# Kernel tuning notes

Hardware: AMD Instinct MI355X
Metric: run time of the kernel (lower is better)

Reference implementation:

```python
import jax, jax.numpy as jnp
import numpy as np
import math

H = 2048        # hidden_size
I = 8192        # intermediate_size
NH = 16         # num_heads
NKV = 4         # num_kv_heads
HD = 128        # head_dim
RD = 128        # rope_dim
THETA = 1000000.0
C = 8192        # context_length
EPS = 1e-6


def setup_inputs() -> dict:
    key = jax.random.key(0)
    ks = jax.random.split(key, 12)
    s = 0.02
    w = lambda k, shape: jax.random.normal(k, shape, jnp.float32) * s
    inp = {
        "hidden_states": jax.random.normal(ks[0], (1, 1, H), jnp.float32),
        "current_pos": jnp.array([4000], dtype=jnp.int32),
        "causal_mask": jnp.zeros((1, 1, 1, C), jnp.float32),
        "Wq": w(ks[1], (NH * HD * 2, H)),
        "Wk": w(ks[2], (NKV * HD, H)),
        "Wv": w(ks[3], (NKV * HD, H)),
        "Wo": w(ks[4], (H, NH * HD)),
        "q_norm": jnp.ones((HD,), jnp.float32),
        "k_norm": jnp.ones((HD,), jnp.float32),
        "ln1_w": jnp.ones((H,), jnp.float32),
        "ln2_w": jnp.ones((H,), jnp.float32),
        "W_gate": w(ks[5], (I, H)),
        "W_up": w(ks[6], (I, H)),
        "W_down": w(ks[7], (H, I)),
        "kv_cache": jax.random.normal(ks[8], (2, NKV, C, HD), jnp.float32) * 0.5,
    }
    inv_freq = 1.0 / (THETA ** (jnp.arange(0, RD, 2, dtype=jnp.float32) / RD))
    freqs = jnp.arange(C, dtype=jnp.float32)[:, None] * inv_freq[None, :]  # [C, RD/2]
    inp["rope_cos"] = jnp.cos(freqs)
    inp["rope_sin"] = jnp.sin(freqs)
    return inp


def _rms(x, w):
    return x * jax.lax.rsqrt(jnp.mean(x * x, axis=-1, keepdims=True) + EPS) * w


def _rope(x, cos, sin):
    # x: [heads, head_dim]; cos/sin: [RD/2]
    half = RD // 2
    x1, x2, xp = x[:, :half], x[:, half:RD], x[:, RD:]
    return jnp.concatenate([x1 * cos - x2 * sin, x2 * cos + x1 * sin, xp], axis=-1)


def reference(hidden_states, current_pos, causal_mask, Wq, Wk, Wv, Wo,
              q_norm, k_norm, ln1_w, ln2_w, W_gate, W_up, W_down,
              kv_cache, rope_cos, rope_sin):
    residual = hidden_states
    h = _rms(hidden_states, ln1_w)[0, 0]                  # [H]
    qg = (Wq @ h).reshape(NH, 2 * HD)
    q, gate = qg[:, :HD], qg[:, HD:]
    k = (Wk @ h).reshape(NKV, HD)
    v = (Wv @ h).reshape(NKV, HD)
    q = _rms(q, q_norm)
    k = _rms(k, k_norm)
    p = current_pos[0]
    cos, sin = rope_cos[p], rope_sin[p]
    q = _rope(q, cos, sin)
    k = _rope(k, cos, sin)
    z = jnp.int32(0)
    kc = jax.lax.dynamic_update_slice(kv_cache[0], k[:, None, :], (z, p, z))  # [NKV, C, HD]
    vc = jax.lax.dynamic_update_slice(kv_cache[1], v[:, None, :], (z, p, z))
    groups = NH // NKV
    k_exp = jnp.repeat(kc, groups, axis=0)                # [NH, C, HD]
    v_exp = jnp.repeat(vc, groups, axis=0)
    scale = 1.0 / math.sqrt(HD)
    scores = jnp.einsum('hd,hcd->hc', q, k_exp) * scale + causal_mask.reshape(1, C)
    attn = jax.nn.softmax(scores, axis=-1)
    attn_out = jnp.einsum('hc,hcd->hd', attn, v_exp) * jax.nn.sigmoid(gate)
    out = (Wo @ attn_out.reshape(NH * HD)).reshape(1, 1, H)
    x = residual + out
    h2 = _rms(x, ln2_w)
    ffn = (jax.nn.silu(h2 @ W_gate.T) * (h2 @ W_up.T)) @ W_down.T
    return x + ffn
```

## Files before the change

### kernel.cpp

```cpp
#include <hip/hip_runtime.h>

#define H 2048
#define NH 16
#define NKV 4
#define HD 128
#define CTX 8192
#define IDIM 8192
#define EPS 1e-6f
#define SCALE 0.08838834764831845f

__device__ __forceinline__ float wave_sum(float x){
#pragma unroll
    for(int o=32;o>0;o>>=1) x += __shfl_xor(x,o,64);
    return x;
}
__device__ __forceinline__ float wave_max(float x){
#pragma unroll
    for(int o=32;o>0;o>>=1) x = fmaxf(x,__shfl_xor(x,o,64));
    return x;
}
__device__ __forceinline__ void keep4(const float4& v){
    asm volatile("" :: "v"(v.x), "v"(v.y), "v"(v.z), "v"(v.w));
}
__device__ __forceinline__ void stage16(const float* g, float* l){
    __builtin_amdgcn_global_load_lds(
        (const __attribute__((address_space(1))) void*)g,
        (__attribute__((address_space(3))) void*)l, 16, 0, 0);
}

__global__ __launch_bounds__(512) void k_qkv(const float* __restrict__ Wq,
                                             const float* __restrict__ Wk,
                                             const float* __restrict__ Wv,
                                             const float* __restrict__ hs,
                                             const float* __restrict__ ln1,
                                             float* __restrict__ qg,
                                             float* __restrict__ kvec,
                                             float* __restrict__ vvec){
    __shared__ __align__(16) float hw[H];
    __shared__ __align__(16) float wlds[8*2048];
    __shared__ float red[8];
    int tid = threadIdx.x, wid = tid>>6, lane = tid&63;
    int row = blockIdx.x*8 + wid;
    const float* wr; float* op;
    if(row < 4096)      { wr = Wq + (size_t)row*H;        op = qg   + row; }
    else if(row < 4608) { wr = Wk + (size_t)(row-4096)*H; op = kvec + (row-4096); }
    else                { wr = Wv + (size_t)(row-4608)*H; op = vvec + (row-4608); }
    float4 a  = *(const float4*)(hs  + tid*4);
    float4 wa = *(const float4*)(ln1 + tid*4);
#pragma unroll
    for(int i=0;i<8;i++) stage16(wr + i*256 + lane*4, wlds + wid*2048 + i*256);

    float ss = a.x*a.x + a.y*a.y + a.z*a.z + a.w*a.w;
    ss = wave_sum(ss);
    if(lane==0) red[wid] = ss;
    __syncthreads();
    float tot = red[0]+red[1]+red[2]+red[3]+red[4]+red[5]+red[6]+red[7];
    float rs = rsqrtf(tot/(float)H + EPS);
    *(float4*)(hw + tid*4) = make_float4(a.x*rs*wa.x, a.y*rs*wa.y, a.z*rs*wa.z, a.w*rs*wa.w);
    __syncthreads();

    float acc = 0.f;
#pragma unroll
    for(int i=0;i<8;i++){
        float4 rv = *(const float4*)(wlds + wid*2048 + i*256 + lane*4);
        float4 hv = *(const float4*)(hw + i*256 + lane*4);
        acc += rv.x*hv.x + rv.y*hv.y + rv.z*hv.z + rv.w*hv.w;
    }
    acc = wave_sum(acc);
    if(lane==0) *op = acc;
}

__global__ __launch_bounds__(64) void k_rope(const float* __restrict__ qg,
                                             const float* __restrict__ kvec,
                                             const float* __restrict__ vvec,
                                             const int* __restrict__ pos,
                                             const float* __restrict__ qn,
                                             const float* __restrict__ kn,
                                             const float* __restrict__ rc,
                                             const float* __restrict__ rsn,
                                             float* __restrict__ q_rope,
                                             float* __restrict__ gate_sig,
                                             float* __restrict__ knew,
                                             float* __restrict__ vnew){
    int b = blockIdx.x, lane = threadIdx.x;
    int p = pos[0];
    float c = rc[(size_t)p*64 + lane];
    float s = rsn[(size_t)p*64 + lane];
    if(b < NH){
        int h = b;
        float x1 = qg[h*256 + lane], x2 = qg[h*256 + 64 + lane];
        float ssq = wave_sum(x1*x1 + x2*x2);
        float r = rsqrtf(ssq/128.f + EPS);
        float n1 = x1*r*qn[lane];
        float n2 = x2*r*qn[lane+64];
        q_rope[h*128 + lane]      = n1*c - n2*s;
        q_rope[h*128 + 64 + lane] = n2*c + n1*s;
        float g1 = qg[h*256 + 128 + lane], g2 = qg[h*256 + 192 + lane];
        gate_sig[h*128 + lane]      = 1.f/(1.f + __expf(-g1));
        gate_sig[h*128 + 64 + lane] = 1.f/(1.f + __expf(-g2));
    } else {
        int j = b - NH;
        float x1 = kvec[j*128 + lane], x2 = kvec[j*128 + 64 + lane];
        float ssq = wave_sum(x1*x1 + x2*x2);
        float r = rsqrtf(ssq/128.f + EPS);
        float n1 = x1*r*kn[lane];
        float n2 = x2*r*kn[lane+64];
        knew[j*128 + lane]      = n1*c - n2*s;
        knew[j*128 + 64 + lane] = n2*c + n1*s;
        vnew[j*128 + lane]      = vvec[j*128 + lane];
        vnew[j*128 + 64 + lane] = vvec[j*128 + 64 + lane];
    }
}

__global__ __launch_bounds__(128) void k_attn_part(const float* __restrict__ cache,
                                                   const float* __restrict__ q_rope,
                                                   const float* __restrict__ mask,
                                                   const int* __restrict__ pos,
                                                   const float* __restrict__ knew,
                                                   const float* __restrict__ vnew,
                                                   float* __restrict__ part_m,
                                                   float* __restrict__ part_l,
                                                   float* __restrict__ part_o,
                                                   int nchunk, int chunk){
    int j = blockIdx.y, ci = blockIdx.x, tid = threadIdx.x;
    int p = pos[0];
    __shared__ float q_s[512];
    __shared__ float s_s[512];
    __shared__ float m_s[4], l_s[4], mt_s[4], lt_s[4];
#pragma unroll
    for(int t=0;t<4;t++) q_s[t*128 + tid] = q_rope[j*512 + t*128 + tid];
    if(tid < 4){ m_s[tid] = -3.0e38f; l_s[tid] = 0.f; }
    float o0=0.f,o1=0.f,o2=0.f,o3=0.f;
    __syncthreads();
    int base0 = ci*chunk;
    for(int s0=0; s0<chunk; s0+=128){
        int c = base0 + s0 + tid;
        const float* kr = (c==p) ? (knew + (size_t)j*HD)
                                 : (cache + ((size_t)j*CTX + c)*HD);
        float a0=0.f,a1=0.f,a2=0.f,a3=0.f;
        for(int d0=0; d0<HD; d0+=32){
            float4 u8[8];
#pragma unroll
            for(int t=0;t<8;t++) u8[t] = *(const float4*)(kr + d0 + t*4);
#pragma unroll
            for(int t=0;t<8;t++) keep4(u8[t]);
#pragma unroll
            for(int t=0;t<8;t++){
                int dd = d0 + t*4;
                const float* q0=q_s+dd; const float* q1=q_s+128+dd;
                const float* q2=q_s+256+dd; const float* q3=q_s+384+dd;
                a0 += q0[0]*u8[t].x+q0[1]*u8[t].y+q0[2]*u8[t].z+q0[3]*u8[t].w;
                a1 += q1[0]*u8[t].x+q1[1]*u8[t].y+q1[2]*u8[t].z+q1[3]*u8[t].w;
                a2 += q2[0]*u8[t].x+q2[1]*u8[t].y+q2[2]*u8[t].z+q2[3]*u8[t].w;
                a3 += q3[0]*u8[t].x+q3[1]*u8[t].y+q3[2]*u8[t].z+q3[3]*u8[t].w;
            }
        }
        float mv = mask[c];
        s_s[tid]       = a0*SCALE + mv;
        s_s[128 + tid] = a1*SCALE + mv;
        s_s[256 + tid] = a2*SCALE + mv;
        s_s[384 + tid] = a3*SCALE + mv;
        __syncthreads();
        int wid = tid>>6, lane = tid&63;
#pragma unroll
        for(int hh=0; hh<2; hh++){
            int h = wid*2 + hh;
            float v0 = s_s[h*128 + lane], v1 = s_s[h*128 + 64 + lane];
            float m = wave_max(fmaxf(v0, v1));
            float l = wave_sum(__expf(v0 - m) + __expf(v1 - m));
            if(lane==0){ mt_s[h]=m; lt_s[h]=l; }
        }
        __syncthreads();
        float mn[4], sc_old[4];
#pragma unroll
        for(int h=0;h<4;h++){
            mn[h] = fmaxf(m_s[h], mt_s[h]);
            sc_old[h] = __expf(m_s[h] - mn[h]);
        }
        float w0 = __expf(s_s[tid]       - mn[0]);
        float w1 = __expf(s_s[128 + tid] - mn[1]);
        float w2 = __expf(s_s[256 + tid] - mn[2]);
        float w3 = __expf(s_s[384 + tid] - mn[3]);
        __syncthreads();
        s_s[tid]=w0; s_s[128+tid]=w1; s_s[256+tid]=w2; s_s[384+tid]=w3;
        if(tid < 4){
            l_s[tid] = l_s[tid]*sc_old[tid] + lt_s[tid]*__expf(mt_s[tid] - mn[tid]);
            m_s[tid] = mn[tid];
        }
        __syncthreads();
        o0 *= sc_old[0]; o1 *= sc_old[1]; o2 *= sc_old[2]; o3 *= sc_old[3];
        const float* vb = cache + (size_t)NKV*CTX*HD + ((size_t)j*CTX + base0 + s0)*HD;
        for(int cc0=0; cc0<128; cc0+=16){
            float v[16];
#pragma unroll
            for(int t=0;t<16;t++){
                int gpos = base0 + s0 + cc0 + t;
                const float* vrow = (gpos==p) ? (vnew + (size_t)j*HD)
                                              : (vb + (size_t)(cc0+t)*HD);
                v[t] = vrow[tid];
            }
            asm volatile("" :: "v"(v[0]),  "v"(v[1]),  "v"(v[2]),  "v"(v[3]),
                              "v"(v[4]),  "v"(v[5]),  "v"(v[6]),  "v"(v[7]),
                              "v"(v[8]),  "v"(v[9]),  "v"(v[10]), "v"(v[11]),
                              "v"(v[12]), "v"(v[13]), "v"(v[14]), "v"(v[15]));
#pragma unroll
            for(int t=0;t<16;t++){
                int cc = cc0 + t;
                o0 += s_s[cc]*v[t];
                o1 += s_s[128+cc]*v[t];
                o2 += s_s[256+cc]*v[t];
                o3 += s_s[384+cc]*v[t];
            }
        }
        __syncthreads();
    }
    int h0 = j*4;
    part_o[((size_t)(h0+0)*nchunk + ci)*128 + tid] = o0;
    part_o[((size_t)(h0+1)*nchunk + ci)*128 + tid] = o1;
    part_o[((size_t)(h0+2)*nchunk + ci)*128 + tid] = o2;
    part_o[((size_t)(h0+3)*nchunk + ci)*128 + tid] = o3;
    if(tid < 4){
        part_m[(h0+tid)*nchunk + ci] = m_s[tid];
        part_l[(h0+tid)*nchunk + ci] = l_s[tid];
    }
}

__global__ __launch_bounds__(128) void k_attn_red(const float* __restrict__ part_m,
                                                  const float* __restrict__ part_l,
                                                  const float* __restrict__ part_o,
                                                  const float* __restrict__ gate_sig,
                                                  float* __restrict__ attn,
                                                  int nchunk){
    __shared__ float e_s[64];
    __shared__ float lg_s;
    int h = blockIdx.x, tid = threadIdx.x, lane = tid&63, w = tid>>6;
    if(w == 0){
        float pm = (lane < nchunk) ? part_m[h*nchunk + lane] : -3.0e38f;
        float pl = (lane < nchunk) ? part_l[h*nchunk + lane] : 0.f;
        float mg = wave_max(pm);
        float e  = (lane < nchunk) ? __expf(pm - mg) : 0.f;
        float lg = wave_sum(pl * e);
        if(lane < 64) e_s[lane] = e;
        if(lane == 0) lg_s = lg;
    }
    __syncthreads();
    float lg = lg_s;
    float oa = 0.f;
    for(int i=0;i<nchunk;i++)
        oa += e_s[i]*part_o[((size_t)h*nchunk + i)*128 + tid];
    attn[h*128 + tid] = oa/lg * gate_sig[h*128 + tid];
}

__global__ __launch_bounds__(512) void k_wo(const float* __restrict__ Wo,
                                            const float* __restrict__ attn,
                                            const float* __restrict__ resid,
                                            float* __restrict__ x){
    __shared__ __align__(16) float wlds[8*2048];
    int tid = threadIdx.x, wid = tid>>6, lane = tid&63;
    int row = blockIdx.x*8 + wid;
    const float* wr = Wo + (size_t)row*H;
    float4 hv[8];
#pragma unroll
    for(int i=0;i<8;i++) hv[i] = *(const float4*)(attn + i*256 + lane*4);
#pragma unroll
    for(int i=0;i<8;i++) stage16(wr + i*256 + lane*4, wlds + wid*2048 + i*256);
    __syncthreads();
    float acc = 0.f;
#pragma unroll
    for(int i=0;i<8;i++){
        float4 rv = *(const float4*)(wlds + wid*2048 + i*256 + lane*4);
        acc += rv.x*hv[i].x + rv.y*hv[i].y + rv.z*hv[i].z + rv.w*hv[i].w;
    }
    acc = wave_sum(acc);
    if(lane==0) x[row] = resid[row] + acc;
}

__global__ __launch_bounds__(512) void k_gateup(const float* __restrict__ Wg,
                                                const float* __restrict__ Wu,
                                                const float* __restrict__ xres,
                                                const float* __restrict__ ln2,
                                                float* __restrict__ act){
    __shared__ __align__(16) float hw[H];
    __shared__ __align__(16) float wlds[8*2048];
    __shared__ float red[8];
    int tid = threadIdx.x, wid = tid>>6, lane = tid&63;
    int row = blockIdx.x*8 + wid;
    const float* gr = Wg + (size_t)row*H;
    const float* ur = Wu + (size_t)row*H;
    float4 a  = *(const float4*)(xres + (size_t)tid*4);
    float4 wa = *(const float4*)(ln2  + (size_t)tid*4);
#pragma unroll
    for(int i=0;i<8;i++) stage16(gr + i*256 + lane*4, wlds + wid*2048 + i*256);

    float ss = a.x*a.x + a.y*a.y + a.z*a.z + a.w*a.w;
    ss = wave_sum(ss);
    if(lane==0) red[wid] = ss;
    __syncthreads();
    float tot = red[0]+red[1]+red[2]+red[3]+red[4]+red[5]+red[6]+red[7];
    float rs = rsqrtf(tot/(float)H + EPS);
    *(float4*)(hw + tid*4) = make_float4(a.x*rs*wa.x, a.y*rs*wa.y, a.z*rs*wa.z, a.w*rs*wa.w);
    __syncthreads();

    float ag = 0.f;
#pragma unroll
    for(int i=0;i<8;i++){
        float4 gv = *(const float4*)(wlds + wid*2048 + i*256 + lane*4);
        float4 hv = *(const float4*)(hw + i*256 + lane*4);
        ag += gv.x*hv.x + gv.y*hv.y + gv.z*hv.z + gv.w*hv.w;
    }
    ag = wave_sum(ag);
    __syncthreads();
#pragma unroll
    for(int i=0;i<8;i++) stage16(ur + i*256 + lane*4, wlds + wid*2048 + i*256);
    __syncthreads();

    float au = 0.f;
#pragma unroll
    for(int i=0;i<8;i++){
        float4 uv = *(const float4*)(wlds + wid*2048 + i*256 + lane*4);
        float4 hv = *(const float4*)(hw + i*256 + lane*4);
        au += uv.x*hv.x + uv.y*hv.y + uv.z*hv.z + uv.w*hv.w;
    }
    au = wave_sum(au);
    if(lane==0){
        float sg = ag/(1.f + __expf(-ag));
        act[row] = sg*au;
    }
}

__global__ __launch_bounds__(256,2) void k_down(const float* __restrict__ Wd,
                                                const float* __restrict__ act,
                                                const float* __restrict__ x,
                                                float* __restrict__ out){
    __shared__ __align__(16) float wlds[4*4096];
    __shared__ float part[4];
    int tid = threadIdx.x, wid = tid>>6, lane = tid&63;
    int row  = blockIdx.x*2 + (wid>>1);
    int half = wid&1;
    const float* wr = Wd + (size_t)row*IDIM + half*4096;
#pragma unroll
    for(int i=0;i<16;i++) stage16(wr + i*256 + lane*4, wlds + wid*4096 + i*256);
    __syncthreads();
    float acc = 0.f;
#pragma unroll
    for(int i=0;i<16;i++){
        float4 rv = *(const float4*)(wlds + wid*4096 + i*256 + lane*4);
        float4 av = *(const float4*)(act + half*4096 + i*256 + lane*4);
        acc += rv.x*av.x + rv.y*av.y + rv.z*av.z + rv.w*av.w;
    }
    acc = wave_sum(acc);
    if(lane==0) part[wid] = acc;
    __syncthreads();
    if(tid < 2){
        int rr = blockIdx.x*2 + tid;
        out[rr] = x[rr] + part[tid*2] + part[tid*2+1];
    }
}

extern "C" void kernel_launch(void* const* d_in, const int* in_sizes, int n_in,
                              void* d_out, int out_size, void* d_ws, size_t ws_size,
                              hipStream_t stream){
    const float* hs   = (const float*)d_in[0];
    const int*   pos  = (const int*)d_in[1];
    const float* mask = (const float*)d_in[2];
    const float* Wq   = (const float*)d_in[3];
    const float* Wk   = (const float*)d_in[4];
    const float* Wv   = (const float*)d_in[5];
    const float* Wo   = (const float*)d_in[6];
    const float* qn   = (const float*)d_in[7];
    const float* kn   = (const float*)d_in[8];
    const float* ln1  = (const float*)d_in[9];
    const float* ln2  = (const float*)d_in[10];
    const float* Wg   = (const float*)d_in[11];
    const float* Wu   = (const float*)d_in[12];
    const float* Wd   = (const float*)d_in[13];
    const float* cache= (const float*)d_in[14];
    const float* rc   = (const float*)d_in[15];
    const float* rsn  = (const float*)d_in[16];
    float* out = (float*)d_out;

    float* ws       = (float*)d_ws;
    float* qg       = ws;
    float* kvec     = ws + 4096;
    float* vvec     = ws + 4608;
    float* q_rope   = ws + 5120;
    float* gate_sig = ws + 7168;
    float* xres     = ws + 9216;
    float* attn     = ws + 15360;
    float* act      = ws + 17408;
    float* knew     = ws + 25600;
    float* vnew     = ws + 26112;
    int nchunk = 64;
    while(nchunk > 1){
        size_t need = (size_t)(26624 + 2*NH*nchunk + (size_t)NH*nchunk*128) * 4;
        if(need <= ws_size) break;
        nchunk >>= 1;
    }
    int chunk = CTX / nchunk;
    float* part_m = ws + 26624;
    float* part_l = part_m + NH*nchunk;
    float* part_o = part_l + NH*nchunk;

    k_qkv<<<576,512,0,stream>>>(Wq, Wk, Wv, hs, ln1, qg, kvec, vvec);
    k_rope<<<20,64,0,stream>>>(qg, kvec, vvec, pos, qn, kn, rc, rsn, q_rope, gate_sig, knew, vnew);
    dim3 g3(nchunk, NKV);
    k_attn_part<<<g3,128,0,stream>>>(cache, q_rope, mask, pos, knew, vnew,
                                     part_m, part_l, part_o, nchunk, chunk);
    k_attn_red<<<16,128,0,stream>>>(part_m, part_l, part_o, gate_sig, attn, nchunk);
    k_wo<<<256,512,0,stream>>>(Wo, attn, hs, xres);
    k_gateup<<<1024,512,0,stream>>>(Wg, Wu, xres, ln2, act);
    k_down<<<1024,256,0,stream>>>(Wd, act, xres, out);
}
```

Before: 309.9 us.

## Specialize attention waves to stage V into LDS, and co-stage gate/up rows

The attention partial kernel doubles its block to 256 threads. Two waves compute QK scores while the other two stage the V tile into a 64KB LDS buffer, and all four waves then split the PV accumulation across row halves before a final LDS reduction. The gate/up kernel now has each 4-wave block issue the gate and up row loads together before the RMSNorm, which removes a barrier and serial staging phase. The cost is much larger LDS use per block, which can limit occupancy, and half the attention waves sit idle during the score phase.

Result: no change. 305.8 us (-1.3%).

```diff
diff --git a/kernel.cpp b/kernel.cpp
--- a/kernel.cpp
+++ b/kernel.cpp
@@ -112,7 +112,7 @@
     }
 }
 
-__global__ __launch_bounds__(128) void k_attn_part(const float* __restrict__ cache,
+__global__ __launch_bounds__(256) void k_attn_part(const float* __restrict__ cache,
                                                    const float* __restrict__ q_rope,
                                                    const float* __restrict__ mask,
                                                    const int* __restrict__ pos,
@@ -124,104 +124,106 @@
                                                    int nchunk, int chunk){
     int j = blockIdx.y, ci = blockIdx.x, tid = threadIdx.x;
     int p = pos[0];
-    __shared__ float q_s[512];
+    __shared__ __align__(16) float q_s[512];
     __shared__ float s_s[512];
-    __shared__ float m_s[4], l_s[4], mt_s[4], lt_s[4];
-#pragma unroll
-    for(int t=0;t<4;t++) q_s[t*128 + tid] = q_rope[j*512 + t*128 + tid];
+    __shared__ __align__(16) float V_s[128*128];
+    __shared__ float m_s[4], l_s[4], sc_s[4];
+    int lane = tid&63, w = tid>>6;
+    int base0 = ci*chunk;
+
+    q_s[tid]       = q_rope[j*512 + tid];
+    q_s[256 + tid] = q_rope[j*512 + 256 + tid];
     if(tid < 4){ m_s[tid] = -3.0e38f; l_s[tid] = 0.f; }
     float o0=0.f,o1=0.f,o2=0.f,o3=0.f;
     __syncthreads();
-    int base0 = ci*chunk;
+
     for(int s0=0; s0<chunk; s0+=128){
-        int c = base0 + s0 + tid;
-        const float* kr = (c==p) ? (knew + (size_t)j*HD)
-                                 : (cache + ((size_t)j*CTX + c)*HD);
-        float a0=0.f,a1=0.f,a2=0.f,a3=0.f;
-        for(int d0=0; d0<HD; d0+=32){
-            float4 u8[8];
-#pragma unroll
-            for(int t=0;t<8;t++) u8[t] = *(const float4*)(kr + d0 + t*4);
-#pragma unroll
-            for(int t=0;t<8;t++) keep4(u8[t]);
-#pragma unroll
-            for(int t=0;t<8;t++){
-                int dd = d0 + t*4;
-                const float* q0=q_s+dd; const float* q1=q_s+128+dd;
-                const float* q2=q_s+256+dd; const float* q3=q_s+384+dd;
-                a0 += q0[0]*u8[t].x+q0[1]*u8[t].y+q0[2]*u8[t].z+q0[3]*u8[t].w;
-                a1 += q1[0]*u8[t].x+q1[1]*u8[t].y+q1[2]*u8[t].z+q1[3]*u8[t].w;
-                a2 += q2[0]*u8[t].x+q2[1]*u8[t].y+q2[2]*u8[t].z+q2[3]*u8[t].w;
-                a3 += q3[0]*u8[t].x+q3[1]*u8[t].y+q3[2]*u8[t].z+q3[3]*u8[t].w;
+        if(w >= 2){
+            const float* vb = cache + (size_t)NKV*CTX*HD + ((size_t)j*CTX + base0 + s0)*HD;
+            int half = w - 2;
+#pragma unroll
+            for(int i=0;i<32;i++){
+                int idx = half*32 + i;
+                stage16(vb + idx*256 + lane*4, V_s + idx*256);
             }
-        }
-        float mv = mask[c];
-        s_s[tid]       = a0*SCALE + mv;
-        s_s[128 + tid] = a1*SCALE + mv;
-        s_s[256 + tid] = a2*SCALE + mv;
-        s_s[384 + tid] = a3*SCALE + mv;
-        __syncthreads();
-        int wid = tid>>6, lane = tid&63;
-#pragma unroll
-        for(int hh=0; hh<2; hh++){
-            int h = wid*2 + hh;
-            float v0 = s_s[h*128 + lane], v1 = s_s[h*128 + 64 + lane];
-            float m = wave_max(fmaxf(v0, v1));
-            float l = wave_sum(__expf(v0 - m) + __expf(v1 - m));
-            if(lane==0){ mt_s[h]=m; lt_s[h]=l; }
+        } else {
+            int c = base0 + s0 + tid;
+            const float* kr = (c==p) ? (knew + (size_t)j*HD)
+                                     : (cache + ((size_t)j*CTX + c)*HD);
+            float a0=0.f,a1=0.f,a2=0.f,a3=0.f;
+            for(int d0=0; d0<HD; d0+=32){
+                float4 u8[8];
+#pragma unroll
+                for(int t=0;t<8;t++) u8[t] = *(const float4*)(kr + d0 + t*4);
+#pragma unroll
+                for(int t=0;t<8;t++) keep4(u8[t]);
+#pragma unroll
+                for(int t=0;t<8;t++){
+                    int dd = d0 + t*4;
+                    const float* q0=q_s+dd; const float* q1=q_s+128+dd;
+                    const float* q2=q_s+256+dd; const float* q3=q_s+384+dd;
+                    a0 += q0[0]*u8[t].x+q0[1]*u8[t].y+q0[2]*u8[t].z+q0[3]*u8[t].w;
+                    a1 += q1[0]*u8[t].x+q1[1]*u8[t].y+q1[2]*u8[t].z+q1[3]*u8[t].w;
+                    a2 += q2[0]*u8[t].x+q2[1]*u8[t].y+q2[2]*u8[t].z+q2[3]*u8[t].w;
+                    a3 += q3[0]*u8[t].x+q3[1]*u8[t].y+q3[2]*u8[t].z+q3[3]*u8[t].w;
+                }
+            }
+            float mv = mask[c];
+            s_s[tid]       = a0*SCALE + mv;
+            s_s[128 + tid] = a1*SCALE + mv;
+            s_s[256 + tid] = a2*SCALE + mv;
+            s_s[384 + tid] = a3*SCALE + mv;
         }
         __syncthreads();
-        float mn[4], sc_old[4];
-#pragma unroll
-        for(int h=0;h<4;h++){
-            mn[h] = fmaxf(m_s[h], mt_s[h]);
-            sc_old[h] = __expf(m_s[h] - mn[h]);
-        }
-        float w0 = __expf(s_s[tid]       - mn[0]);
-        float w1 = __expf(s_s[128 + tid] - mn[1]);
-        float w2 = __expf(s_s[256 + tid] - mn[2]);
-        float w3 = __expf(s_s[384 + tid] - mn[3]);
-        __syncthreads();
-        s_s[tid]=w0; s_s[128+tid]=w1; s_s[256+tid]=w2; s_s[384+tid]=w3;
-        if(tid < 4){
-            l_s[tid] = l_s[tid]*sc_old[tid] + lt_s[tid]*__expf(mt_s[tid] - mn[tid]);
-            m_s[tid] = mn[tid];
+
+        int prow = p - (base0 + s0);
+        if(prow >= 0 && prow < 128 && tid < 128)
+            V_s[prow*128 + tid] = vnew[(size_t)j*HD + tid];
+
+        {
+            float v0 = s_s[w*128 + lane], v1 = s_s[w*128 + 64 + lane];
+            float mt = wave_max(fmaxf(v0, v1));
+            float mn = fmaxf(m_s[w], mt);
+            float sc = __expf(m_s[w] - mn);
+            float w0 = __expf(v0 - mn), w1 = __expf(v1 - mn);
+            float lt = wave_sum(w0 + w1);
+            s_s[w*128 + lane]      = w0;
+            s_s[w*128 + 64 + lane] = w1;
+            if(lane==0){ l_s[w] = l_s[w]*sc + lt; m_s[w] = mn; sc_s[w] = sc; }
         }
         __syncthreads();
-        o0 *= sc_old[0]; o1 *= sc_old[1]; o2 *= sc_old[2]; o3 *= sc_old[3];
-        const float* vb = cache + (size_t)NKV*CTX*HD + ((size_t)j*CTX + base0 + s0)*HD;
-        for(int cc0=0; cc0<128; cc0+=16){
-            float v[16];
-#pragma unroll
-            for(int t=0;t<16;t++){
-                int gpos = base0 + s0 + cc0 + t;
-                const float* vrow = (gpos==p) ? (vnew + (size_t)j*HD)
-                                              : (vb + (size_t)(cc0+t)*HD);
-                v[t] = vrow[tid];
-            }
-            asm volatile("" :: "v"(v[0]),  "v"(v[1]),  "v"(v[2]),  "v"(v[3]),
-                              "v"(v[4]),  "v"(v[5]),  "v"(v[6]),  "v"(v[7]),
-                              "v"(v[8]),  "v"(v[9]),  "v"(v[10]), "v"(v[11]),
-                              "v"(v[12]), "v"(v[13]), "v"(v[14]), "v"(v[15]));
-#pragma unroll
-            for(int t=0;t<16;t++){
-                int cc = cc0 + t;
-                o0 += s_s[cc]*v[t];
-                o1 += s_s[128+cc]*v[t];
-                o2 += s_s[256+cc]*v[t];
-                o3 += s_s[384+cc]*v[t];
-            }
+
+        o0 *= sc_s[0]; o1 *= sc_s[1]; o2 *= sc_s[2]; o3 *= sc_s[3];
+        int d = tid & 127, rh = tid >> 7;
+        const float* vbase = V_s + rh*64*128 + d;
+        const float* p0 = s_s + rh*64;
+#pragma unroll 8
+        for(int cc=0; cc<64; cc++){
+            float v = vbase[cc*128];
+            o0 += p0[cc]*v;
+            o1 += p0[128+cc]*v;
+            o2 += p0[256+cc]*v;
+            o3 += p0[384+cc]*v;
         }
         __syncthreads();
     }
-    int h0 = j*4;
-    part_o[((size_t)(h0+0)*nchunk + ci)*128 + tid] = o0;
-    part_o[((size_t)(h0+1)*nchunk + ci)*128 + tid] = o1;
-    part_o[((size_t)(h0+2)*nchunk + ci)*128 + tid] = o2;
-    part_o[((size_t)(h0+3)*nchunk + ci)*128 + tid] = o3;
+
+    int d = tid & 127, rh = tid >> 7;
+    V_s[rh*512 + 0*128 + d] = o0;
+    V_s[rh*512 + 1*128 + d] = o1;
+    V_s[rh*512 + 2*128 + d] = o2;
+    V_s[rh*512 + 3*128 + d] = o3;
+    __syncthreads();
+    if(tid < 128){
+#pragma unroll
+        for(int h=0;h<4;h++){
+            float o = V_s[h*128 + tid] + V_s[512 + h*128 + tid];
+            part_o[((size_t)(j*4+h)*nchunk + ci)*128 + tid] = o;
+        }
+    }
     if(tid < 4){
-        part_m[(h0+tid)*nchunk + ci] = m_s[tid];
-        part_l[(h0+tid)*nchunk + ci] = l_s[tid];
+        part_m[(j*4+tid)*nchunk + ci] = m_s[tid];
+        part_l[(j*4+tid)*nchunk + ci] = l_s[tid];
     }
 }
 
@@ -275,52 +277,50 @@
     if(lane==0) x[row] = resid[row] + acc;
 }
 
-__global__ __launch_bounds__(512) void k_gateup(const float* __restrict__ Wg,
-                                                const float* __restrict__ Wu,
-                                                const float* __restrict__ xres,
-                                                const float* __restrict__ ln2,
-                                                float* __restrict__ act){
+__global__ __launch_bounds__(256,2) void k_gateup(const float* __restrict__ Wg,
+                                                  const float* __restrict__ Wu,
+                                                  const float* __restrict__ xres,
+                                                  const float* __restrict__ ln2,
+                                                  float* __restrict__ act){
     __shared__ __align__(16) float hw[H];
-    __shared__ __align__(16) float wlds[8*2048];
-    __shared__ float red[8];
+    __shared__ __align__(16) float wlds[4*4096];
+    __shared__ float red[4];
     int tid = threadIdx.x, wid = tid>>6, lane = tid&63;
-    int row = blockIdx.x*8 + wid;
+    int row = blockIdx.x*4 + wid;
     const float* gr = Wg + (size_t)row*H;
     const float* ur = Wu + (size_t)row*H;
-    float4 a  = *(const float4*)(xres + (size_t)tid*4);
-    float4 wa = *(const float4*)(ln2  + (size_t)tid*4);
-#pragma unroll
-    for(int i=0;i<8;i++) stage16(gr + i*256 + lane*4, wlds + wid*2048 + i*256);
-
-    float ss = a.x*a.x + a.y*a.y + a.z*a.z + a.w*a.w;
+    float4 a = *(const float4*)(xres + (size_t)tid*8);
+    float4 b = *(const float4*)(xres + (size_t)tid*8 + 4);
+    float4 wa = *(const float4*)(ln2 + (size_t)tid*8);
+    float4 wb = *(const float4*)(ln2 + (size_t)tid*8 + 4);
+#pragma unroll
+    for(int i=0;i<8;i++) stage16(gr + i*256 + lane*4, wlds + wid*4096 + i*256);
+#pragma unroll
+    for(int i=0;i<8;i++) stage16(ur + i*256 + lane*4, wlds + wid*4096 + 2048 + i*256);
+
+    float x[8] = {a.x,a.y,a.z,a.w,b.x,b.y,b.z,b.w};
+    float ss = 0.f;
+#pragma unroll
+    for(int i=0;i<8;i++) ss += x[i]*x[i];
     ss = wave_sum(ss);
     if(lane==0) red[wid] = ss;
     __syncthreads();
-    float tot = red[0]+red[1]+red[2]+red[3]+red[4]+red[5]+red[6]+red[7];
+    float tot = red[0]+red[1]+red[2]+red[3];
     float rs = rsqrtf(tot/(float)H + EPS);
-    *(float4*)(hw + tid*4) = make_float4(a.x*rs*wa.x, a.y*rs*wa.y, a.z*rs*wa.z, a.w*rs*wa.w);
-    __syncthreads();
-
-    float ag = 0.f;
+    *(float4*)(hw + tid*8)     = make_float4(x[0]*rs*wa.x, x[1]*rs*wa.y, x[2]*rs*wa.z, x[3]*rs*wa.w);
+    *(float4*)(hw + tid*8 + 4) = make_float4(x[4]*rs*wb.x, x[5]*rs*wb.y, x[6]*rs*wb.z, x[7]*rs*wb.w);
+    __syncthreads();
+
+    float ag = 0.f, au = 0.f;
 #pragma unroll
     for(int i=0;i<8;i++){
-        float4 gv = *(const float4*)(wlds + wid*2048 + i*256 + lane*4);
+        float4 gv = *(const float4*)(wlds + wid*4096 + i*256 + lane*4);
+        float4 uv = *(const float4*)(wlds + wid*4096 + 2048 + i*256 + lane*4);
         float4 hv = *(const float4*)(hw + i*256 + lane*4);
         ag += gv.x*hv.x + gv.y*hv.y + gv.z*hv.z + gv.w*hv.w;
+        au += uv.x*hv.x + uv.y*hv.y + uv.z*hv.z + uv.w*hv.w;
     }
     ag = wave_sum(ag);
-    __syncthreads();
-#pragma unroll
-    for(int i=0;i<8;i++) stage16(ur + i*256 + lane*4, wlds + wid*2048 + i*256);
-    __syncthreads();
-
-    float au = 0.f;
-#pragma unroll
-    for(int i=0;i<8;i++){
-        float4 uv = *(const float4*)(wlds + wid*2048 + i*256 + lane*4);
-        float4 hv = *(const float4*)(hw + i*256 + lane*4);
-        au += uv.x*hv.x + uv.y*hv.y + uv.z*hv.z + uv.w*hv.w;
-    }
     au = wave_sum(au);
     if(lane==0){
         float sg = ag/(1.f + __expf(-ag));
@@ -404,10 +404,10 @@
     k_qkv<<<576,512,0,stream>>>(Wq, Wk, Wv, hs, ln1, qg, kvec, vvec);
     k_rope<<<20,64,0,stream>>>(qg, kvec, vvec, pos, qn, kn, rc, rsn, q_rope, gate_sig, knew, vnew);
     dim3 g3(nchunk, NKV);
-    k_attn_part<<<g3,128,0,stream>>>(cache, q_rope, mask, pos, knew, vnew,
+    k_attn_part<<<g3,256,0,stream>>>(cache, q_rope, mask, pos, knew, vnew,
                                      part_m, part_l, part_o, nchunk, chunk);
     k_attn_red<<<16,128,0,stream>>>(part_m, part_l, part_o, gate_sig, attn, nchunk);
     k_wo<<<256,512,0,stream>>>(Wo, attn, hs, xres);
-    k_gateup<<<1024,512,0,stream>>>(Wg, Wu, xres, ln2, act);
+    k_gateup<<<2048,256,0,stream>>>(Wg, Wu, xres, ln2, act);
     k_down<<<1024,256,0,stream>>>(Wd, act, xres, out);
 }
```
